# Kernel optimization log

Hardware: AMD Instinct MI355X
Metric: run time of the kernel (lower is better)

## Reference

```python
import jax, jax.numpy as jnp
import numpy as np

N, E, IN, HID, H, OUT, G = 50000, 800000, 128, 64, 4, 40, 8
D = HID * H  # 256, concat-head feature dim
NEG_SLOPE = 0.2
EPS = 1e-5


def setup_inputs() -> dict:
    key = jax.random.key(0)
    ks = iter(jax.random.split(key, 40))
    def w(shape, s=0.05):
        return jax.random.normal(next(ks), shape, jnp.float32) * s
    inp = {
        "x": jax.random.normal(next(ks), (N, IN), jnp.float32),
        "edge_index": jax.random.randint(next(ks), (2, E), 0, N),
        "batch": jnp.sort(jax.random.randint(next(ks), (N,), 0, G)),
        # encoder MLP (depth 1): Linear -> LayerNorm -> ReLU -> Linear
        "enc_w1": w((IN, HID)), "enc_b1": jnp.zeros(HID),
        "enc_g": jnp.ones(HID), "enc_be": jnp.zeros(HID),
        "enc_w2": w((HID, HID)), "enc_b2": jnp.zeros(HID),
        # GAT layer 0: in=HID, out=HID, heads=H
        "conv0_w": w((HID, D)), "conv0_as": w((H, HID)), "conv0_ad": w((H, HID)), "conv0_b": jnp.zeros(D),
        # GAT layer 1: in=D, out=HID, heads=H
        "conv1_w": w((D, D)), "conv1_as": w((H, HID)), "conv1_ad": w((H, HID)), "conv1_b": jnp.zeros(D),
        # GAT layer 2 (appended, use_dec=True): in=D, out=HID, heads=H
        "conv2_w": w((D, D)), "conv2_as": w((H, HID)), "conv2_ad": w((H, HID)), "conv2_b": jnp.zeros(D),
        # decoder MLP: Linear -> LayerNorm -> ReLU -> Linear
        "dec_w1": w((D, HID)), "dec_b1": jnp.zeros(HID),
        "dec_g": jnp.ones(HID), "dec_be": jnp.zeros(HID),
        "dec_w2": w((HID, OUT)), "dec_b2": jnp.zeros(OUT),
    }
    return inp


def layernorm(x, g, b):
    m = jnp.mean(x, -1, keepdims=True)
    v = jnp.mean(jnp.square(x - m), -1, keepdims=True)
    return g * (x - m) * jax.lax.rsqrt(v + EPS) + b


def gat_layer(x, src, dst, W, a_src, a_dst, bias):
    # x: [N, F_in]; PyG GATConv with add_self_loops (src/dst already include them)
    h = (x @ W).reshape(N, H, HID)                      # [N, H, C]
    al_s = jnp.einsum('nhc,hc->nh', h, a_src)           # [N, H]
    al_d = jnp.einsum('nhc,hc->nh', h, a_dst)
    e = al_s[src] + al_d[dst]                           # [E', H]
    e = jnp.where(e > 0, e, NEG_SLOPE * e)              # leaky_relu
    m = jax.ops.segment_max(e, dst, num_segments=N)     # per-target softmax
    e = jnp.exp(e - m[dst])
    s = jax.ops.segment_sum(e, dst, num_segments=N)
    alpha = e / (s[dst] + 1e-16)                        # [E', H]
    out = jax.ops.segment_sum(h[src] * alpha[:, :, None], dst, num_segments=N)
    return out.reshape(N, D) + bias                     # concat heads + bias


def reference(x, edge_index, batch,
              enc_w1, enc_b1, enc_g, enc_be, enc_w2, enc_b2,
              conv0_w, conv0_as, conv0_ad, conv0_b,
              conv1_w, conv1_as, conv1_ad, conv1_b,
              conv2_w, conv2_as, conv2_ad, conv2_b,
              dec_w1, dec_b1, dec_g, dec_be, dec_w2, dec_b2):
    loop = jnp.arange(N, dtype=edge_index.dtype)
    src = jnp.concatenate([edge_index[0], loop])
    dst = jnp.concatenate([edge_index[1], loop])
    # encoder MLP
    h = jax.nn.relu(layernorm(x @ enc_w1 + enc_b1, enc_g, enc_be)) @ enc_w2 + enc_b2
    # stacked GAT layers, each followed by ELU
    for (W, a_s, a_d, b) in ((conv0_w, conv0_as, conv0_ad, conv0_b),
                             (conv1_w, conv1_as, conv1_ad, conv1_b),
                             (conv2_w, conv2_as, conv2_ad, conv2_b)):
        h = jax.nn.elu(gat_layer(h, src, dst, W, a_s, a_d, b))
    # global mean pool
    sums = jax.ops.segment_sum(h, batch, num_segments=G)          # [G, D]
    cnt = jax.ops.segment_sum(jnp.ones((N, 1), h.dtype), batch, num_segments=G)
    pooled = sums / jnp.maximum(cnt, 1.0)
    # decoder MLP
    out = jax.nn.relu(layernorm(pooled @ dec_w1 + dec_b1, dec_g, dec_be)) @ dec_w2 + dec_b2
    return out
```

## Files before the change

### kernel.cpp

```cpp
#include <hip/hip_runtime.h>
#include <hip/hip_bf16.h>

#define N_NODES 50000
#define E_EDGES 800000
#define IN_F 128
#define HIDF 64
#define HEADS 4
#define OUT_F 40
#define GROUPS 8
#define D_F 256
#define NEG 0.2f
#define LNEPS 1e-5f
#define POOL_CHUNK 128
#define POOL_BLOCKS ((N_NODES + POOL_CHUNK - 1) / POOL_CHUNK)
#define NB256 ((N_NODES + 255) / 256)

#define OFF_X    0
#define OFF_EW1  6400000
#define OFF_EB1  6408192
#define OFF_EG   6408256
#define OFF_EBE  6408320
#define OFF_EW2  6408384
#define OFF_EB2  6412480
#define OFF_C0W  6412544
#define OFF_C0AS 6428928
#define OFF_C0AD 6429184
#define OFF_C0B  6429440
#define OFF_C1W  6429696
#define OFF_C1AS 6495232
#define OFF_C1AD 6495488
#define OFF_C1B  6495744
#define OFF_C2W  6496000
#define OFF_C2AS 6561536
#define OFF_C2AD 6561792
#define OFF_C2B  6562048
#define OFF_DW1  6562304
#define OFF_DB1  6578688
#define OFF_DG   6578752
#define OFF_DBE  6578816
#define OFF_DW2  6578880
#define OFF_DB2  6581440
#define CANON_TOT 6581480

__device__ __constant__ int c_off[26] = {
    OFF_X, OFF_EW1, OFF_EB1, OFF_EG, OFF_EBE, OFF_EW2, OFF_EB2,
    OFF_C0W, OFF_C0AS, OFF_C0AD, OFF_C0B,
    OFF_C1W, OFF_C1AS, OFF_C1AD, OFF_C1B,
    OFF_C2W, OFF_C2AS, OFF_C2AD, OFF_C2B,
    OFF_DW1, OFF_DB1, OFF_DG, OFF_DBE, OFF_DW2, OFF_DB2, CANON_TOT};

typedef __attribute__((ext_vector_type(8))) short bf16x8;
typedef __attribute__((ext_vector_type(4))) float f32x4;

__device__ __forceinline__ float bf2f(unsigned short u) {
    union { unsigned int i; float f; } v; v.i = ((unsigned int)u) << 16; return v.f;
}
__device__ __forceinline__ unsigned short f2bf(float f) {
    union { float f; unsigned int i; } v; v.f = f;
    unsigned int r = v.i + 0x7FFF + ((v.i >> 16) & 1);
    return (unsigned short)(r >> 16);
}
__device__ __forceinline__ void mac8(float* acc, float w, uint4 u) {
    acc[0] = fmaf(w, bf2f((unsigned short)(u.x & 0xffff)), acc[0]);
    acc[1] = fmaf(w, bf2f((unsigned short)(u.x >> 16)),    acc[1]);
    acc[2] = fmaf(w, bf2f((unsigned short)(u.y & 0xffff)), acc[2]);
    acc[3] = fmaf(w, bf2f((unsigned short)(u.y >> 16)),    acc[3]);
    acc[4] = fmaf(w, bf2f((unsigned short)(u.z & 0xffff)), acc[4]);
    acc[5] = fmaf(w, bf2f((unsigned short)(u.z >> 16)),    acc[5]);
    acc[6] = fmaf(w, bf2f((unsigned short)(u.w & 0xffff)), acc[6]);
    acc[7] = fmaf(w, bf2f((unsigned short)(u.w >> 16)),    acc[7]);
}
__device__ __forceinline__ int dtype_flag(const unsigned short* encg) {
    return (encg[0] == 0x0000 && encg[1] == 0x3F80) ? 1 : 0;
}

struct SP { const void* q[25]; };
__global__ __launch_bounds__(256) void convert_k(SP sp, unsigned short* __restrict__ canon) {
    int i = blockIdx.x * 256 + threadIdx.x;
    if (i >= CANON_TOT) return;
    int fl = dtype_flag((const unsigned short*)sp.q[3]);
    if (i < OFF_EW1) {
        canon[i] = fl == 0 ? ((const unsigned short*)sp.q[0])[i]
                           : f2bf(((const float*)sp.q[0])[i]);
        return;
    }
    int t = 1;
    while (i >= c_off[t + 1]) ++t;
    int j = i - c_off[t];
    const void* s = sp.q[t];
    canon[i] = fl == 0 ? ((const unsigned short*)s)[j] : f2bf(((const float*)s)[j]);
}

__global__ void wt_k(const unsigned short* __restrict__ canon,
                     unsigned short* __restrict__ wt0, unsigned short* __restrict__ wt1,
                     unsigned short* __restrict__ wt2, unsigned short* __restrict__ w1t,
                     unsigned short* __restrict__ w2t, unsigned short* __restrict__ p0) {
    int i = blockIdx.x * 256 + threadIdx.x;
    if (i < 8192) {
        int k = i >> 6, n = i & 63;
        w1t[n * 128 + k] = canon[OFF_EW1 + k * 64 + n];
    }
    if (i < 4096) {
        int k = i >> 6, n = i & 63;
        w2t[n * 64 + k] = canon[OFF_EW2 + k * 64 + n];
    }
    if (i < 16384) {
        int k = i >> 8, n = i & 255;
        wt0[n * 64 + k] = canon[OFF_C0W + i];
    }
    if (i < 65536) {
        int k = i >> 8, n = i & 255;
        wt1[n * 256 + k] = canon[OFF_C1W + i];
        wt2[n * 256 + k] = canon[OFF_C2W + i];
    }
    if (i < 512) {
        int out = i & 7, k = i >> 3;
        int h = out & 3, sd = out >> 2;
        int abase = (sd == 0 ? OFF_C0AS : OFF_C0AD) + h * 64;
        int wbase = OFF_C0W + k * 256 + h * 64;
        float s = 0.f;
        for (int c = 0; c < 64; ++c)
            s = fmaf(bf2f(canon[wbase + c]), bf2f(canon[abase + c]), s);
        p0[k * 8 + out] = f2bf(s);
    }
}

__global__ __launch_bounds__(128) void enc1_k(const unsigned short* __restrict__ canon,
                                              const unsigned short* __restrict__ w1t,
                                              unsigned short* __restrict__ T1) {
    const unsigned short* x = canon + OFF_X;
    __shared__ unsigned short As[128 * 72];
    __shared__ unsigned short Bs[64 * 72];
    int tid = threadIdx.x, wave = tid >> 6, lane = tid & 63;
    int q = lane >> 4, l = lane & 15;
    int row0 = blockIdx.x * 128;
    f32x4 acc[4][4];
#pragma unroll
    for (int a = 0; a < 4; ++a)
#pragma unroll
        for (int b = 0; b < 4; ++b) acc[a][b] = (f32x4){0.f, 0.f, 0.f, 0.f};
    for (int kb = 0; kb < IN_F; kb += 64) {
#pragma unroll
        for (int it = 0; it < 8; ++it) {
            int cid = it * 128 + tid;
            int r = cid >> 3, kc = cid & 7;
            int gr = row0 + r;
            uint4 v = make_uint4(0, 0, 0, 0);
            if (gr < N_NODES) v = *(const uint4*)(x + (size_t)gr * IN_F + kb + kc * 8);
            *(uint4*)&As[r * 72 + kc * 8] = v;
        }
#pragma unroll
        for (int it = 0; it < 4; ++it) {
            int cid = it * 128 + tid;
            int r = cid >> 3, kc = cid & 7;
            uint4 w = *(const uint4*)(w1t + (size_t)r * IN_F + kb + kc * 8);
            *(uint4*)&Bs[r * 72 + kc * 8] = w;
        }
        __syncthreads();
#pragma unroll
        for (int ks = 0; ks < 64; ks += 32) {
            bf16x8 af[4], bfr[4];
#pragma unroll
            for (int mt = 0; mt < 4; ++mt)
                af[mt] = *(const bf16x8*)&As[(wave * 64 + mt * 16 + l) * 72 + ks + q * 8];
#pragma unroll
            for (int nt = 0; nt < 4; ++nt)
                bfr[nt] = *(const bf16x8*)&Bs[(nt * 16 + l) * 72 + ks + q * 8];
#pragma unroll
            for (int mt = 0; mt < 4; ++mt)
#pragma unroll
                for (int nt = 0; nt < 4; ++nt)
                    acc[mt][nt] = __builtin_amdgcn_mfma_f32_16x16x32_bf16(
                        af[mt], bfr[nt], acc[mt][nt], 0, 0, 0);
        }
        __syncthreads();
    }
    float b1c[4], gc[4], bec[4];
#pragma unroll
    for (int nt = 0; nt < 4; ++nt) {
        int c = nt * 16 + l;
        b1c[nt] = bf2f(canon[OFF_EB1 + c]);
        gc[nt]  = bf2f(canon[OFF_EG + c]);
        bec[nt] = bf2f(canon[OFF_EBE + c]);
    }
#pragma unroll
    for (int mt = 0; mt < 4; ++mt) {
#pragma unroll
        for (int r = 0; r < 4; ++r) {
            int grow = row0 + wave * 64 + mt * 16 + q * 4 + r;
            float v0 = acc[mt][0][r] + b1c[0];
            float v1 = acc[mt][1][r] + b1c[1];
            float v2 = acc[mt][2][r] + b1c[2];
            float v3 = acc[mt][3][r] + b1c[3];
            float s = v0 + v1 + v2 + v3;
#pragma unroll
            for (int off = 1; off < 16; off <<= 1) s += __shfl_xor(s, off);
            float mean = s * (1.0f / 64.0f);
            float d0 = v0 - mean, d1 = v1 - mean, d2 = v2 - mean, d3 = v3 - mean;
            float vs = d0 * d0 + d1 * d1 + d2 * d2 + d3 * d3;
#pragma unroll
            for (int off = 1; off < 16; off <<= 1) vs += __shfl_xor(vs, off);
            float rstd = rsqrtf(vs * (1.0f / 64.0f) + LNEPS);
            if (grow < N_NODES) {
                unsigned short* trow = T1 + (size_t)grow * HIDF;
                float o0 = gc[0] * d0 * rstd + bec[0]; o0 = fmaxf(o0, 0.f);
                float o1 = gc[1] * d1 * rstd + bec[1]; o1 = fmaxf(o1, 0.f);
                float o2 = gc[2] * d2 * rstd + bec[2]; o2 = fmaxf(o2, 0.f);
                float o3 = gc[3] * d3 * rstd + bec[3]; o3 = fmaxf(o3, 0.f);
                trow[l] = f2bf(o0); trow[16 + l] = f2bf(o1);
                trow[32 + l] = f2bf(o2); trow[48 + l] = f2bf(o3);
            }
        }
    }
}

__global__ __launch_bounds__(128) void enc2_k(const unsigned short* __restrict__ canon,
                                              const unsigned short* __restrict__ T1,
                                              const unsigned short* __restrict__ w2t,
                                              const unsigned short* __restrict__ p0,
                                              unsigned short* __restrict__ h0,
                                              float* __restrict__ alS, float* __restrict__ alD) {
    __shared__ unsigned short As[128 * 72];
    __shared__ unsigned short Bs[64 * 72];
    int tid = threadIdx.x, wave = tid >> 6, lane = tid & 63;
    int q = lane >> 4, l = lane & 15;
    int row0 = blockIdx.x * 128;
    f32x4 acc[4][4];
#pragma unroll
    for (int a = 0; a < 4; ++a)
#pragma unroll
        for (int b = 0; b < 4; ++b) acc[a][b] = (f32x4){0.f, 0.f, 0.f, 0.f};
#pragma unroll
    for (int it = 0; it < 8; ++it) {
        int cid = it * 128 + tid;
        int r = cid >> 3, kc = cid & 7;
        int gr = row0 + r;
        uint4 v = make_uint4(0, 0, 0, 0);
        if (gr < N_NODES) v = *(const uint4*)(T1 + (size_t)gr * HIDF + kc * 8);
        *(uint4*)&As[r * 72 + kc * 8] = v;
    }
#pragma unroll
    for (int it = 0; it < 4; ++it) {
        int cid = it * 128 + tid;
        int r = cid >> 3, kc = cid & 7;
        uint4 w = *(const uint4*)(w2t + (size_t)r * HIDF + kc * 8);
        *(uint4*)&Bs[r * 72 + kc * 8] = w;
    }
    __syncthreads();
#pragma unroll
    for (int ks = 0; ks < 64; ks += 32) {
        bf16x8 af[4], bfr[4];
#pragma unroll
        for (int mt = 0; mt < 4; ++mt)
            af[mt] = *(const bf16x8*)&As[(wave * 64 + mt * 16 + l) * 72 + ks + q * 8];
#pragma unroll
        for (int nt = 0; nt < 4; ++nt)
            bfr[nt] = *(const bf16x8*)&Bs[(nt * 16 + l) * 72 + ks + q * 8];
#pragma unroll
        for (int mt = 0; mt < 4; ++mt)
#pragma unroll
            for (int nt = 0; nt < 4; ++nt)
                acc[mt][nt] = __builtin_amdgcn_mfma_f32_16x16x32_bf16(
                    af[mt], bfr[nt], acc[mt][nt], 0, 0, 0);
    }
    float b2c[4];
#pragma unroll
    for (int nt = 0; nt < 4; ++nt) b2c[nt] = bf2f(canon[OFF_EB2 + nt * 16 + l]);
    __syncthreads();
#pragma unroll
    for (int mt = 0; mt < 4; ++mt) {
#pragma unroll
        for (int r = 0; r < 4; ++r) {
            int lr = wave * 64 + mt * 16 + q * 4 + r;
#pragma unroll
            for (int nt = 0; nt < 4; ++nt)
                As[lr * 72 + nt * 16 + l] = f2bf(acc[mt][nt][r] + b2c[nt]);
        }
    }
    float* p0f = (float*)Bs;
    for (int i = tid; i < 512; i += 128) p0f[i] = bf2f(p0[i]);
    __syncthreads();
    int row = tid, grow = row0 + row;
    if (grow < N_NODES) {
        const unsigned short* srow = &As[row * 72];
        unsigned short* hrow = h0 + (size_t)grow * HIDF;
#pragma unroll
        for (int i = 0; i < 8; ++i)
            *(uint4*)(hrow + i * 8) = *(const uint4*)(srow + i * 8);
        float s[8] = {};
#pragma unroll
        for (int k = 0; k < 64; ++k) {
            float hv = bf2f(srow[k]);
            const float* pp = &p0f[k * 8];
#pragma unroll
            for (int o = 0; o < 8; ++o) s[o] = fmaf(hv, pp[o], s[o]);
        }
#pragma unroll
        for (int h = 0; h < 4; ++h) {
            alS[(size_t)grow * 4 + h] = s[h];
            alD[(size_t)grow * 4 + h] = s[4 + h];
        }
    }
}

__global__ void deg_init_k(int* __restrict__ deg) {
    int i = blockIdx.x * 256 + threadIdx.x;
    if (i < N_NODES) deg[i] = 1;
}
__global__ void deg_count_k(const int* __restrict__ dstI, int* __restrict__ deg) {
    int i = blockIdx.x * 256 + threadIdx.x;
    if (i < E_EDGES) atomicAdd(&deg[dstI[i]], 1);
}
__global__ __launch_bounds__(256) void scan1_k(const int* __restrict__ deg, int* __restrict__ excl,
                                               int* __restrict__ bsums) {
    int tid = threadIdx.x, lane = tid & 63, wv = tid >> 6;
    int gid = blockIdx.x * 256 + tid;
    int v = (gid < N_NODES) ? deg[gid] : 0;
    int inc = v;
#pragma unroll
    for (int off = 1; off < 64; off <<= 1) { int t = __shfl_up(inc, off); if (lane >= off) inc += t; }
    __shared__ int wsum[4];
    if (lane == 63) wsum[wv] = inc;
    __syncthreads();
    int wo = 0;
    for (int w = 0; w < wv; ++w) wo += wsum[w];
    int incl = inc + wo;
    if (gid < N_NODES) excl[gid] = incl - v;
    if (tid == 255) bsums[blockIdx.x] = incl;
}
__global__ __launch_bounds__(256) void scan2_k(const int* __restrict__ bsums, int* __restrict__ boff,
                                               int* __restrict__ totalp) {
    int tid = threadIdx.x, lane = tid & 63, wv = tid >> 6;
    int v = (tid < NB256) ? bsums[tid] : 0;
    int inc = v;
#pragma unroll
    for (int off = 1; off < 64; off <<= 1) { int t = __shfl_up(inc, off); if (lane >= off) inc += t; }
    __shared__ int wsum[4];
    if (lane == 63) wsum[wv] = inc;
    __syncthreads();
    int wo = 0;
    for (int w = 0; w < wv; ++w) wo += wsum[w];
    int incl = inc + wo;
    if (tid < NB256) boff[tid] = incl - v;
    if (tid == 255) *totalp = incl;
}
__global__ void scan3_k(const int* __restrict__ excl, const int* __restrict__ boff,
                        int* __restrict__ rowp, int* __restrict__ cursor) {
    int i = blockIdx.x * 256 + threadIdx.x;
    if (i < N_NODES) { int r = excl[i] + boff[i >> 8]; rowp[i] = r; cursor[i] = r; }
}
__global__ void fill_k(const int* __restrict__ srcI, const int* __restrict__ dstI,
                       int* __restrict__ cursor, int* __restrict__ colx) {
    int i = blockIdx.x * 256 + threadIdx.x;
    if (i >= E_EDGES + N_NODES) return;
    int s, d;
    if (i < E_EDGES) { s = srcI[i]; d = dstI[i]; } else { s = i - E_EDGES; d = s; }
    int slot = atomicAdd(&cursor[d], 1);
    colx[slot] = s;
}

__global__ __launch_bounds__(256) void agg0_k(
    const unsigned short* __restrict__ h0, const int* __restrict__ rowp, const int* __restrict__ colx,
    const float* __restrict__ alS, const float* __restrict__ alD,
    unsigned short* __restrict__ z0) {
    int tid = threadIdx.x, wave = tid >> 6, lane = tid & 63;
    int n = blockIdx.x * 4 + wave;
    if (n >= N_NODES) return;
    int start = rowp[n], end = rowp[n + 1];
    int e = lane >> 5;
    int c = lane & 31;
    int head = c >> 3;
    float adh = alD[(size_t)n * 4 + head];
    float a0 = 0.f, a1 = 0.f, asum = 0.f;
    int j = start;
    for (; j + 7 < end; j += 8) {
        int ja = j + e, jb = j + 2 + e, jc2 = j + 4 + e, jd = j + 6 + e;
        int sa = colx[ja], sb = colx[jb], sc = colx[jc2], sd = colx[jd];
        float ea = alS[(size_t)sa * 4 + head] + adh; ea = ea > 0.f ? ea : NEG * ea;
        float eb = alS[(size_t)sb * 4 + head] + adh; eb = eb > 0.f ? eb : NEG * eb;
        float ec = alS[(size_t)sc * 4 + head] + adh; ec = ec > 0.f ? ec : NEG * ec;
        float ed = alS[(size_t)sd * 4 + head] + adh; ed = ed > 0.f ? ed : NEG * ed;
        float wa = __expf(ea), wb = __expf(eb), wc = __expf(ec), wd = __expf(ed);
        unsigned int ua = *(const unsigned int*)(h0 + (size_t)sa * HIDF + c * 2);
        unsigned int ub = *(const unsigned int*)(h0 + (size_t)sb * HIDF + c * 2);
        unsigned int uc = *(const unsigned int*)(h0 + (size_t)sc * HIDF + c * 2);
        unsigned int ud = *(const unsigned int*)(h0 + (size_t)sd * HIDF + c * 2);
        asum += (wa + wb) + (wc + wd);
        a0 = fmaf(wa, bf2f((unsigned short)(ua & 0xffff)), a0);
        a1 = fmaf(wa, bf2f((unsigned short)(ua >> 16)),    a1);
        a0 = fmaf(wb, bf2f((unsigned short)(ub & 0xffff)), a0);
        a1 = fmaf(wb, bf2f((unsigned short)(ub >> 16)),    a1);
        a0 = fmaf(wc, bf2f((unsigned short)(uc & 0xffff)), a0);
        a1 = fmaf(wc, bf2f((unsigned short)(uc >> 16)),    a1);
        a0 = fmaf(wd, bf2f((unsigned short)(ud & 0xffff)), a0);
        a1 = fmaf(wd, bf2f((unsigned short)(ud >> 16)),    a1);
    }
    for (; j < end; j += 2) {
        int j1 = j + e;
        int jc = j1 < end ? j1 : end - 1;
        int s1 = colx[jc];
        float w1 = 0.f;
        if (j1 < end) {
            float ev = alS[(size_t)s1 * 4 + head] + adh;
            ev = ev > 0.f ? ev : NEG * ev;
            w1 = __expf(ev);
        }
        unsigned int u1 = *(const unsigned int*)(h0 + (size_t)s1 * HIDF + c * 2);
        asum += w1;
        a0 = fmaf(w1, bf2f((unsigned short)(u1 & 0xffff)), a0);
        a1 = fmaf(w1, bf2f((unsigned short)(u1 >> 16)),    a1);
    }
    a0 += __shfl_xor(a0, 32);
    a1 += __shfl_xor(a1, 32);
    asum += __shfl_xor(asum, 32);
    if (lane < 32) {
        float rh = 1.f / (asum + 1e-16f);
        unsigned int o = (unsigned int)f2bf(a0 * rh) | ((unsigned int)f2bf(a1 * rh) << 16);
        *(unsigned int*)(z0 + (size_t)n * HIDF + c * 2) = o;
    }
}

__global__ __launch_bounds__(256) void mfma_mm_k(
    const unsigned short* __restrict__ A, const unsigned short* __restrict__ Wt,
    unsigned short* __restrict__ C, int M, int K,
    const unsigned short* __restrict__ bias,
    const unsigned short* __restrict__ aSv, const unsigned short* __restrict__ aDv,
    float* __restrict__ alS, float* __restrict__ alD) {
    __shared__ unsigned short smem[128 * 72 * 2];
    unsigned short* As = smem;
    unsigned short* Bs = smem + 128 * 72;
    int tid = threadIdx.x;
    int wave = tid >> 6, lane = tid & 63;
    int wm = wave >> 1, wn = wave & 1;
    int row0 = blockIdx.y * 128, col0 = blockIdx.x * 128;
    int q = lane >> 4, l = lane & 15;
    f32x4 acc[4][4];
#pragma unroll
    for (int a = 0; a < 4; ++a)
#pragma unroll
        for (int b = 0; b < 4; ++b) acc[a][b] = (f32x4){0.f, 0.f, 0.f, 0.f};
    for (int kb = 0; kb < K; kb += 64) {
#pragma unroll
        for (int it = 0; it < 4; ++it) {
            int cid = it * 256 + tid;
            int r = cid >> 3, kc = cid & 7;
            int gr = row0 + r;
            uint4 v = make_uint4(0, 0, 0, 0);
            if (gr < M) v = *(const uint4*)(A + (size_t)gr * K + kb + kc * 8);
            *(uint4*)&As[r * 72 + kc * 8] = v;
            int gn = col0 + r;
            uint4 w = *(const uint4*)(Wt + (size_t)gn * K + kb + kc * 8);
            *(uint4*)&Bs[r * 72 + kc * 8] = w;
        }
        __syncthreads();
#pragma unroll
        for (int ks = 0; ks < 64; ks += 32) {
            bf16x8 af[4], bfr[4];
#pragma unroll
            for (int mt = 0; mt < 4; ++mt)
                af[mt] = *(const bf16x8*)&As[(wm * 64 + mt * 16 + l) * 72 + ks + q * 8];
#pragma unroll
            for (int nt = 0; nt < 4; ++nt)
                bfr[nt] = *(const bf16x8*)&Bs[(wn * 64 + nt * 16 + l) * 72 + ks + q * 8];
#pragma unroll
            for (int mt = 0; mt < 4; ++mt)
#pragma unroll
                for (int nt = 0; nt < 4; ++nt)
                    acc[mt][nt] = __builtin_amdgcn_mfma_f32_16x16x32_bf16(
                        af[mt], bfr[nt], acc[mt][nt], 0, 0, 0);
        }
        __syncthreads();
    }
    float bv[4] = {0.f, 0.f, 0.f, 0.f};
    bool doBias = (bias != nullptr);
    if (doBias) {
#pragma unroll
        for (int nt = 0; nt < 4; ++nt)
            bv[nt] = bf2f(bias[col0 + wn * 64 + nt * 16 + l]);
    }
#pragma unroll
    for (int mt = 0; mt < 4; ++mt) {
        int rowb = wm * 64 + mt * 16 + q * 4;
#pragma unroll
        for (int r = 0; r < 4; ++r) {
#pragma unroll
            for (int nt = 0; nt < 4; ++nt) {
                float v = acc[mt][nt][r];
                if (doBias) { v += bv[nt]; v = v > 0.f ? v : __expf(v) - 1.f; }
                smem[(rowb + r) * 136 + wn * 64 + nt * 16 + l] = f2bf(v);
            }
        }
    }
    __syncthreads();
    int row = tid >> 1, half = tid & 1;
    int grow = row0 + row;
    if (grow < M) {
        unsigned short* crow = C + (size_t)grow * D_F + col0 + half * 64;
        const unsigned short* srow = &smem[row * 136 + half * 64];
#pragma unroll
        for (int i = 0; i < 8; ++i)
            *(uint4*)(crow + i * 8) = *(const uint4*)(srow + i * 8);
        if (aSv != nullptr) {
            int head = (col0 >> 6) + half;
            const unsigned short* av = aSv + head * 64;
            const unsigned short* dv = aDv + head * 64;
            float ps = 0.f, pd = 0.f;
#pragma unroll
            for (int k = 0; k < 64; ++k) {
                float hv = bf2f(srow[k]);
                ps = fmaf(hv, bf2f(av[k]), ps);
                pd = fmaf(hv, bf2f(dv[k]), pd);
            }
            alS[(size_t)grow * 4 + head] = ps;
            alD[(size_t)grow * 4 + head] = pd;
        }
    }
}

__global__ __launch_bounds__(256) void agg_k(
    const unsigned short* __restrict__ h2, const int* __restrict__ rowp, const int* __restrict__ colx,
    const float* __restrict__ alS, const float* __restrict__ alD,
    const unsigned short* __restrict__ bias, unsigned short* __restrict__ out) {
    int tid = threadIdx.x, wave = tid >> 6, lane = tid & 63;
    int n = blockIdx.x * 4 + wave;
    if (n >= N_NODES) return;
    int start = rowp[n], end = rowp[n + 1];
    int e = lane >> 5;
    int c = lane & 31;
    int head = c >> 3;
    float adh = alD[(size_t)n * 4 + head];
    float acc[8] = {};
    float asum = 0.f;
    int j = start;
    for (; j + 7 < end; j += 8) {
        int ja = j + e, jb = j + 2 + e, jc2 = j + 4 + e, jd = j + 6 + e;
        int sa = colx[ja], sb = colx[jb], sc = colx[jc2], sd = colx[jd];
        float ea = alS[(size_t)sa * 4 + head] + adh; ea = ea > 0.f ? ea : NEG * ea;
        float eb = alS[(size_t)sb * 4 + head] + adh; eb = eb > 0.f ? eb : NEG * eb;
        float ec = alS[(size_t)sc * 4 + head] + adh; ec = ec > 0.f ? ec : NEG * ec;
        float ed = alS[(size_t)sd * 4 + head] + adh; ed = ed > 0.f ? ed : NEG * ed;
        float wa = __expf(ea), wb = __expf(eb), wc = __expf(ec), wd = __expf(ed);
        uint4 ua = *(const uint4*)(h2 + (size_t)sa * D_F + c * 8);
        uint4 ub = *(const uint4*)(h2 + (size_t)sb * D_F + c * 8);
        uint4 uc = *(const uint4*)(h2 + (size_t)sc * D_F + c * 8);
        uint4 ud = *(const uint4*)(h2 + (size_t)sd * D_F + c * 8);
        asum += (wa + wb) + (wc + wd);
        mac8(acc, wa, ua);
        mac8(acc, wb, ub);
        mac8(acc, wc, uc);
        mac8(acc, wd, ud);
    }
    for (; j < end; j += 2) {
        int j1 = j + e;
        int jc = j1 < end ? j1 : end - 1;
        int s1 = colx[jc];
        float w1 = 0.f;
        if (j1 < end) {
            float ev = alS[(size_t)s1 * 4 + head] + adh;
            ev = ev > 0.f ? ev : NEG * ev;
            w1 = __expf(ev);
        }
        uint4 u1 = *(const uint4*)(h2 + (size_t)s1 * D_F + c * 8);
        asum += w1;
        mac8(acc, w1, u1);
    }
#pragma unroll
    for (int k = 0; k < 8; ++k) acc[k] += __shfl_xor(acc[k], 32);
    asum += __shfl_xor(asum, 32);
    if (lane < 32) {
        float rh = 1.f / (asum + 1e-16f);
        uint4 bu = *(const uint4*)(bias + c * 8);
        float b[8];
        b[0] = bf2f((unsigned short)(bu.x & 0xffff)); b[1] = bf2f((unsigned short)(bu.x >> 16));
        b[2] = bf2f((unsigned short)(bu.y & 0xffff)); b[3] = bf2f((unsigned short)(bu.y >> 16));
        b[4] = bf2f((unsigned short)(bu.z & 0xffff)); b[5] = bf2f((unsigned short)(bu.z >> 16));
        b[6] = bf2f((unsigned short)(bu.w & 0xffff)); b[7] = bf2f((unsigned short)(bu.w >> 16));
        unsigned int o[4];
#pragma unroll
        for (int k = 0; k < 4; ++k) {
            float v0 = acc[2 * k] * rh + b[2 * k];
            float v1 = acc[2 * k + 1] * rh + b[2 * k + 1];
            v0 = v0 > 0.f ? v0 : __expf(v0) - 1.f;
            v1 = v1 > 0.f ? v1 : __expf(v1) - 1.f;
            o[k] = (unsigned int)f2bf(v0) | ((unsigned int)f2bf(v1) << 16);
        }
        *(uint4*)(out + (size_t)n * D_F + c * 8) = make_uint4(o[0], o[1], o[2], o[3]);
    }
}

__global__ __launch_bounds__(256) void pool_k(const unsigned short* __restrict__ h,
                                              const int* __restrict__ batch,
                                              float* __restrict__ part, int* __restrict__ pcnt) {
    __shared__ float sums[GROUPS * D_F];
    __shared__ int cnts[GROUPS];
    int tid = threadIdx.x;
    for (int i = tid; i < GROUPS * D_F; i += 256) sums[i] = 0.f;
    if (tid < GROUPS) cnts[tid] = 0;
    __syncthreads();
    int n0 = blockIdx.x * POOL_CHUNK;
    int n1 = n0 + POOL_CHUNK; if (n1 > N_NODES) n1 = N_NODES;
    for (int n = n0; n < n1; ++n) {
        int b = batch[n];
        sums[b * D_F + tid] += bf2f(h[(size_t)n * D_F + tid]);
        if (tid == 0) cnts[b]++;
    }
    __syncthreads();
    float* po = part + (size_t)blockIdx.x * (GROUPS * D_F);
    for (int i = tid; i < GROUPS * D_F; i += 256) po[i] = sums[i];
    if (tid < GROUPS) pcnt[blockIdx.x * GROUPS + tid] = cnts[tid];
}

__global__ __launch_bounds__(256) void reduce_k(const float* __restrict__ part,
                                                const int* __restrict__ pcnt,
                                                float* __restrict__ gsum, int* __restrict__ gcnt) {
    int g = blockIdx.x, c = threadIdx.x;
    float s = 0.f;
    for (int b = 0; b < POOL_BLOCKS; ++b) s += part[(size_t)b * (GROUPS * D_F) + g * D_F + c];
    gsum[g * D_F + c] = s;
    if (threadIdx.x < 64) {
        int lane = threadIdx.x;
        int cn = 0;
        for (int b = lane; b < POOL_BLOCKS; b += 64) cn += pcnt[b * GROUPS + g];
#pragma unroll
        for (int off = 1; off < 64; off <<= 1) cn += __shfl_xor(cn, off);
        if (lane == 0) gcnt[g] = cn;
    }
}

__global__ __launch_bounds__(256) void dec_k(const float* __restrict__ gsum, const int* __restrict__ gcnt,
    const unsigned short* __restrict__ canon, const unsigned short* __restrict__ encg,
    void* __restrict__ outp) {
    const unsigned short* w1 = canon + OFF_DW1;
    const unsigned short* b1 = canon + OFF_DB1;
    const unsigned short* gam = canon + OFF_DG;
    const unsigned short* bet = canon + OFF_DBE;
    const unsigned short* w2 = canon + OFF_DW2;
    const unsigned short* b2 = canon + OFF_DB2;
    int tid = threadIdx.x, grp = blockIdx.x * 4 + (tid >> 6), lane = tid & 63;
    if (grp >= GROUPS) return;
    float inv = 1.0f / fmaxf((float)gcnt[grp], 1.0f);
    float p[4];
#pragma unroll
    for (int i = 0; i < 4; ++i) p[i] = gsum[grp * D_F + i * 64 + lane] * inv;
    float acc = bf2f(b1[lane]);
#pragma unroll
    for (int i = 0; i < 4; ++i)
        for (int k = 0; k < 64; ++k)
            acc = fmaf(__shfl(p[i], k), bf2f(w1[(i * 64 + k) * 64 + lane]), acc);
    float s = acc;
#pragma unroll
    for (int off = 32; off > 0; off >>= 1) s += __shfl_xor(s, off);
    float mean = s * (1.0f / 64.0f);
    float d = acc - mean;
    float vs = d * d;
#pragma unroll
    for (int off = 32; off > 0; off >>= 1) vs += __shfl_xor(vs, off);
    float rstd = rsqrtf(vs * (1.0f / 64.0f) + LNEPS);
    float val = bf2f(gam[lane]) * d * rstd + bf2f(bet[lane]);
    val = val > 0.f ? val : val * 0.f;
    int cl = (lane < OUT_F) ? lane : 0;
    float acc2 = 0.f;
    for (int k = 0; k < 64; ++k) {
        float wv = bf2f(w2[k * OUT_F + cl]);
        acc2 = fmaf(__shfl(val, k), wv, acc2);
    }
    if (lane < OUT_F) {
        float res = acc2 + bf2f(b2[lane]);
        if (dtype_flag(encg) == 0) ((unsigned short*)outp)[grp * OUT_F + lane] = f2bf(res);
        else                       ((float*)outp)[grp * OUT_F + lane] = res;
    }
}

extern "C" void kernel_launch(void* const* d_in, const int* in_sizes, int n_in,
                              void* d_out, int out_size, void* d_ws, size_t ws_size,
                              hipStream_t stream) {
    const int* ei    = (const int*)d_in[1];
    const int* batch = (const int*)d_in[2];

    char* p = (char*)d_ws;
    unsigned short* canon = (unsigned short*)p; p += (size_t)CANON_TOT * 2 + 16;
    unsigned short* bufA = (unsigned short*)p; p += (size_t)N_NODES * D_F * 2;
    unsigned short* bufB = (unsigned short*)p; p += (size_t)N_NODES * D_F * 2;
    unsigned short* zbuf = (unsigned short*)p; p += (size_t)N_NODES * HIDF * 2;
    unsigned short* wt0 = (unsigned short*)p; p += (size_t)64 * 256 * 2;
    unsigned short* wt1 = (unsigned short*)p; p += (size_t)256 * 256 * 2;
    unsigned short* wt2 = (unsigned short*)p; p += (size_t)256 * 256 * 2;
    unsigned short* w1t = (unsigned short*)p; p += (size_t)64 * 128 * 2;
    unsigned short* w2t = (unsigned short*)p; p += (size_t)64 * 64 * 2;
    unsigned short* p0  = (unsigned short*)p; p += (size_t)64 * 8 * 2 + 16;
    float* alS  = (float*)p; p += (size_t)N_NODES * 4 * 4;
    float* alD  = (float*)p; p += (size_t)N_NODES * 4 * 4;
    float* part = (float*)p; p += (size_t)POOL_BLOCKS * GROUPS * D_F * 4;
    int* pcnt   = (int*)p;   p += (size_t)POOL_BLOCKS * GROUPS * 4;
    float* gsum = (float*)p; p += GROUPS * D_F * 4;
    int* gcnt   = (int*)p;   p += 16 * 4;
    int* deg    = (int*)p;   p += (size_t)N_NODES * 4;
    int* excl   = (int*)p;   p += (size_t)N_NODES * 4;
    int* bsums  = (int*)p;   p += 256 * 4;
    int* boff   = (int*)p;   p += 256 * 4;
    int* rowp   = (int*)p;   p += (size_t)(N_NODES + 4) * 4;
    int* cursor = (int*)p;   p += (size_t)N_NODES * 4;
    int* colx   = (int*)p;   p += (size_t)(E_EDGES + N_NODES) * 4;

    const int* srcI = ei;
    const int* dstI = ei + E_EDGES;

    SP sp;
    sp.q[0] = d_in[0];
    for (int t = 1; t < 25; ++t) sp.q[t] = d_in[t + 2];

    int nwb = (N_NODES + 3) / 4;
    int nb128 = (N_NODES + 127) / 128;

    convert_k<<<(CANON_TOT + 255) / 256, 256, 0, stream>>>(sp, canon);
    wt_k<<<256, 256, 0, stream>>>(canon, wt0, wt1, wt2, w1t, w2t, p0);

    enc1_k<<<nb128, 128, 0, stream>>>(canon, w1t, bufB);
    enc2_k<<<nb128, 128, 0, stream>>>(canon, bufB, w2t, p0, bufA, alS, alD);

    deg_init_k<<<NB256, 256, 0, stream>>>(deg);
    deg_count_k<<<(E_EDGES + 255) / 256, 256, 0, stream>>>(dstI, deg);
    scan1_k<<<NB256, 256, 0, stream>>>(deg, excl, bsums);
    scan2_k<<<1, 256, 0, stream>>>(bsums, boff, rowp + N_NODES);
    scan3_k<<<NB256, 256, 0, stream>>>(excl, boff, rowp, cursor);
    fill_k<<<(E_EDGES + N_NODES + 255) / 256, 256, 0, stream>>>(srcI, dstI, cursor, colx);

    dim3 mmg(2, nb128);
    agg0_k<<<nwb, 256, 0, stream>>>(bufA, rowp, colx, alS, alD, zbuf);
    mfma_mm_k<<<mmg, 256, 0, stream>>>(zbuf, wt0, bufB, N_NODES, HIDF,
                                       canon + OFF_C0B, nullptr, nullptr, nullptr, nullptr);
    mfma_mm_k<<<mmg, 256, 0, stream>>>(bufB, wt1, bufA, N_NODES, D_F,
                                       nullptr, canon + OFF_C1AS, canon + OFF_C1AD, alS, alD);
    agg_k<<<nwb, 256, 0, stream>>>(bufA, rowp, colx, alS, alD, canon + OFF_C1B, bufB);
    mfma_mm_k<<<mmg, 256, 0, stream>>>(bufB, wt2, bufA, N_NODES, D_F,
                                       nullptr, canon + OFF_C2AS, canon + OFF_C2AD, alS, alD);
    agg_k<<<nwb, 256, 0, stream>>>(bufA, rowp, colx, alS, alD, canon + OFF_C2B, bufB);

    pool_k<<<POOL_BLOCKS, 256, 0, stream>>>(bufB, batch, part, pcnt);
    reduce_k<<<GROUPS, 256, 0, stream>>>(part, pcnt, gsum, gcnt);
    dec_k<<<2, 256, 0, stream>>>(gsum, gcnt, canon, (const unsigned short*)d_in[5], d_out);
}
```

Baseline: 595.3 us.

## Fuse encoder kernels, merge degree init into convert, restructure pooling

The two encoder GEMM kernels become one kernel that keeps the LayerNorm/ReLU intermediate in shared memory, so the T1 round trip through global memory and one launch are gone. The degree initialisation is folded into the conversion kernel as extra blocks, which removes another launch. The pooling kernel now splits nodes across waves, accumulates runs of the same group in registers with vectorised loads, and flushes them with shared-memory atomics. This replaces the per-node serial shared-memory updates. The cost is more register pressure in the fused encoder and atomic contention in the pool kernel.

```diff
diff --git a/kernel.cpp b/kernel.cpp
--- a/kernel.cpp
+++ b/kernel.cpp
@@ -41,6 +41,7 @@
 #define OFF_DW2  6578880
 #define OFF_DB2  6581440
 #define CANON_TOT 6581480
+#define CONV_BLKS ((CANON_TOT + 255) / 256)
 
 __device__ __constant__ int c_off[26] = {
     OFF_X, OFF_EW1, OFF_EB1, OFF_EG, OFF_EBE, OFF_EW2, OFF_EB2,
@@ -75,7 +76,13 @@
 }
 
 struct SP { const void* q[25]; };
-__global__ __launch_bounds__(256) void convert_k(SP sp, unsigned short* __restrict__ canon) {
+__global__ __launch_bounds__(256) void convert_k(SP sp, unsigned short* __restrict__ canon,
+                                                 int* __restrict__ deg) {
+    if (blockIdx.x >= CONV_BLKS) {
+        int i = (blockIdx.x - CONV_BLKS) * 256 + threadIdx.x;
+        if (i < N_NODES) deg[i] = 1;
+        return;
+    }
     int i = blockIdx.x * 256 + threadIdx.x;
     if (i >= CANON_TOT) return;
     int fl = dtype_flag((const unsigned short*)sp.q[3]);
@@ -125,9 +132,12 @@
     }
 }
 
-__global__ __launch_bounds__(128) void enc1_k(const unsigned short* __restrict__ canon,
-                                              const unsigned short* __restrict__ w1t,
-                                              unsigned short* __restrict__ T1) {
+__global__ __launch_bounds__(128) void enc_k(const unsigned short* __restrict__ canon,
+                                             const unsigned short* __restrict__ w1t,
+                                             const unsigned short* __restrict__ w2t,
+                                             const unsigned short* __restrict__ p0,
+                                             unsigned short* __restrict__ h0,
+                                             float* __restrict__ alS, float* __restrict__ alD) {
     const unsigned short* x = canon + OFF_X;
     __shared__ unsigned short As[128 * 72];
     __shared__ unsigned short Bs[64 * 72];
@@ -187,7 +197,7 @@
     for (int mt = 0; mt < 4; ++mt) {
 #pragma unroll
         for (int r = 0; r < 4; ++r) {
-            int grow = row0 + wave * 64 + mt * 16 + q * 4 + r;
+            int lr = wave * 64 + mt * 16 + q * 4 + r;
             float v0 = acc[mt][0][r] + b1c[0];
             float v1 = acc[mt][1][r] + b1c[1];
             float v2 = acc[mt][2][r] + b1c[2];
@@ -201,43 +211,15 @@
 #pragma unroll
             for (int off = 1; off < 16; off <<= 1) vs += __shfl_xor(vs, off);
             float rstd = rsqrtf(vs * (1.0f / 64.0f) + LNEPS);
-            if (grow < N_NODES) {
-                unsigned short* trow = T1 + (size_t)grow * HIDF;
-                float o0 = gc[0] * d0 * rstd + bec[0]; o0 = fmaxf(o0, 0.f);
-                float o1 = gc[1] * d1 * rstd + bec[1]; o1 = fmaxf(o1, 0.f);
-                float o2 = gc[2] * d2 * rstd + bec[2]; o2 = fmaxf(o2, 0.f);
-                float o3 = gc[3] * d3 * rstd + bec[3]; o3 = fmaxf(o3, 0.f);
-                trow[l] = f2bf(o0); trow[16 + l] = f2bf(o1);
-                trow[32 + l] = f2bf(o2); trow[48 + l] = f2bf(o3);
-            }
-        }
-    }
-}
-
-__global__ __launch_bounds__(128) void enc2_k(const unsigned short* __restrict__ canon,
-                                              const unsigned short* __restrict__ T1,
-                                              const unsigned short* __restrict__ w2t,
-                                              const unsigned short* __restrict__ p0,
-                                              unsigned short* __restrict__ h0,
-                                              float* __restrict__ alS, float* __restrict__ alD) {
-    __shared__ unsigned short As[128 * 72];
-    __shared__ unsigned short Bs[64 * 72];
-    int tid = threadIdx.x, wave = tid >> 6, lane = tid & 63;
-    int q = lane >> 4, l = lane & 15;
-    int row0 = blockIdx.x * 128;
-    f32x4 acc[4][4];
-#pragma unroll
-    for (int a = 0; a < 4; ++a)
-#pragma unroll
-        for (int b = 0; b < 4; ++b) acc[a][b] = (f32x4){0.f, 0.f, 0.f, 0.f};
-#pragma unroll
-    for (int it = 0; it < 8; ++it) {
-        int cid = it * 128 + tid;
-        int r = cid >> 3, kc = cid & 7;
-        int gr = row0 + r;
-        uint4 v = make_uint4(0, 0, 0, 0);
-        if (gr < N_NODES) v = *(const uint4*)(T1 + (size_t)gr * HIDF + kc * 8);
-        *(uint4*)&As[r * 72 + kc * 8] = v;
+            float o0 = gc[0] * d0 * rstd + bec[0]; o0 = fmaxf(o0, 0.f);
+            float o1 = gc[1] * d1 * rstd + bec[1]; o1 = fmaxf(o1, 0.f);
+            float o2 = gc[2] * d2 * rstd + bec[2]; o2 = fmaxf(o2, 0.f);
+            float o3 = gc[3] * d3 * rstd + bec[3]; o3 = fmaxf(o3, 0.f);
+            As[lr * 72 + l] = f2bf(o0);
+            As[lr * 72 + 16 + l] = f2bf(o1);
+            As[lr * 72 + 32 + l] = f2bf(o2);
+            As[lr * 72 + 48 + l] = f2bf(o3);
+        }
     }
 #pragma unroll
     for (int it = 0; it < 4; ++it) {
@@ -247,6 +229,11 @@
         *(uint4*)&Bs[r * 72 + kc * 8] = w;
     }
     __syncthreads();
+    f32x4 acc2[4][4];
+#pragma unroll
+    for (int a = 0; a < 4; ++a)
+#pragma unroll
+        for (int b = 0; b < 4; ++b) acc2[a][b] = (f32x4){0.f, 0.f, 0.f, 0.f};
 #pragma unroll
     for (int ks = 0; ks < 64; ks += 32) {
         bf16x8 af[4], bfr[4];
@@ -260,8 +247,8 @@
         for (int mt = 0; mt < 4; ++mt)
 #pragma unroll
             for (int nt = 0; nt < 4; ++nt)
-                acc[mt][nt] = __builtin_amdgcn_mfma_f32_16x16x32_bf16(
-                    af[mt], bfr[nt], acc[mt][nt], 0, 0, 0);
+                acc2[mt][nt] = __builtin_amdgcn_mfma_f32_16x16x32_bf16(
+                    af[mt], bfr[nt], acc2[mt][nt], 0, 0, 0);
     }
     float b2c[4];
 #pragma unroll
@@ -274,7 +261,7 @@
             int lr = wave * 64 + mt * 16 + q * 4 + r;
 #pragma unroll
             for (int nt = 0; nt < 4; ++nt)
-                As[lr * 72 + nt * 16 + l] = f2bf(acc[mt][nt][r] + b2c[nt]);
+                As[lr * 72 + nt * 16 + l] = f2bf(acc2[mt][nt][r] + b2c[nt]);
         }
     }
     float* p0f = (float*)Bs;
@@ -303,10 +290,6 @@
     }
 }
 
-__global__ void deg_init_k(int* __restrict__ deg) {
-    int i = blockIdx.x * 256 + threadIdx.x;
-    if (i < N_NODES) deg[i] = 1;
-}
 __global__ void deg_count_k(const int* __restrict__ dstI, int* __restrict__ deg) {
     int i = blockIdx.x * 256 + threadIdx.x;
     if (i < E_EDGES) atomicAdd(&deg[dstI[i]], 1);
@@ -593,16 +576,39 @@
                                               float* __restrict__ part, int* __restrict__ pcnt) {
     __shared__ float sums[GROUPS * D_F];
     __shared__ int cnts[GROUPS];
-    int tid = threadIdx.x;
+    int tid = threadIdx.x, wave = tid >> 6, lane = tid & 63;
     for (int i = tid; i < GROUPS * D_F; i += 256) sums[i] = 0.f;
     if (tid < GROUPS) cnts[tid] = 0;
     __syncthreads();
-    int n0 = blockIdx.x * POOL_CHUNK;
-    int n1 = n0 + POOL_CHUNK; if (n1 > N_NODES) n1 = N_NODES;
+    int n0 = blockIdx.x * POOL_CHUNK + wave * (POOL_CHUNK / 4);
+    int n1 = n0 + POOL_CHUNK / 4; if (n1 > N_NODES) n1 = N_NODES;
+    float a0 = 0.f, a1 = 0.f, a2 = 0.f, a3 = 0.f;
+    int curb = -1, cnt = 0;
     for (int n = n0; n < n1; ++n) {
         int b = batch[n];
-        sums[b * D_F + tid] += bf2f(h[(size_t)n * D_F + tid]);
-        if (tid == 0) cnts[b]++;
+        if (b != curb) {
+            if (curb >= 0) {
+                atomicAdd(&sums[curb * D_F + lane * 4 + 0], a0);
+                atomicAdd(&sums[curb * D_F + lane * 4 + 1], a1);
+                atomicAdd(&sums[curb * D_F + lane * 4 + 2], a2);
+                atomicAdd(&sums[curb * D_F + lane * 4 + 3], a3);
+                if (lane == 0) atomicAdd(&cnts[curb], cnt);
+            }
+            a0 = a1 = a2 = a3 = 0.f; cnt = 0; curb = b;
+        }
+        uint2 u = *(const uint2*)(h + (size_t)n * D_F + lane * 4);
+        a0 += bf2f((unsigned short)(u.x & 0xffff));
+        a1 += bf2f((unsigned short)(u.x >> 16));
+        a2 += bf2f((unsigned short)(u.y & 0xffff));
+        a3 += bf2f((unsigned short)(u.y >> 16));
+        ++cnt;
+    }
+    if (curb >= 0) {
+        atomicAdd(&sums[curb * D_F + lane * 4 + 0], a0);
+        atomicAdd(&sums[curb * D_F + lane * 4 + 1], a1);
+        atomicAdd(&sums[curb * D_F + lane * 4 + 2], a2);
+        atomicAdd(&sums[curb * D_F + lane * 4 + 3], a3);
+        if (lane == 0) atomicAdd(&cnts[curb], cnt);
     }
     __syncthreads();
     float* po = part + (size_t)blockIdx.x * (GROUPS * D_F);
@@ -712,14 +718,12 @@
     int nwb = (N_NODES + 3) / 4;
     int nb128 = (N_NODES + 127) / 128;
 
-    convert_k<<<(CANON_TOT + 255) / 256, 256, 0, stream>>>(sp, canon);
+    convert_k<<<CONV_BLKS + NB256, 256, 0, stream>>>(sp, canon, deg);
     wt_k<<<256, 256, 0, stream>>>(canon, wt0, wt1, wt2, w1t, w2t, p0);
-
-    enc1_k<<<nb128, 128, 0, stream>>>(canon, w1t, bufB);
-    enc2_k<<<nb128, 128, 0, stream>>>(canon, bufB, w2t, p0, bufA, alS, alD);
-
-    deg_init_k<<<NB256, 256, 0, stream>>>(deg);
     deg_count_k<<<(E_EDGES + 255) / 256, 256, 0, stream>>>(dstI, deg);
+
+    enc_k<<<nb128, 128, 0, stream>>>(canon, w1t, w2t, p0, bufA, alS, alD);
+
     scan1_k<<<NB256, 256, 0, stream>>>(deg, excl, bsums);
     scan2_k<<<1, 256, 0, stream>>>(bsums, boff, rowp + N_NODES);
     scan3_k<<<NB256, 256, 0, stream>>>(excl, boff, rowp, cursor);
```

New measurement: 575.9 us. 3.3% less time.
